# Performance work log

Hardware: AMD Instinct MI355X
Metric: run time of the kernel (lower is better)

Reference implementation:

```python
import jax, jax.numpy as jnp
from jax import lax
import numpy as np

HH = WW = 128          # backbone feature map (2048px image / stride 16)
C_IN = 512
FEAT_STRIDE = 16
N_ANCHOR = 9
NMS_THRESH = 0.7
N_PRE_NMS = 6000
N_POST_NMS = 300
MIN_SIZE = 16
NEG = jnp.float32(-1e30)


def _anchor_base(base_size=16, ratios=(0.5, 1.0, 2.0), scales=(8, 16, 32)):
    py = px = base_size / 2.0
    ab = np.zeros((len(ratios) * len(scales), 4), np.float32)
    for i, r in enumerate(ratios):
        for j, s in enumerate(scales):
            h = base_size * s * np.sqrt(r)
            w = base_size * s * np.sqrt(1.0 / r)
            ab[i * len(scales) + j] = [py - h / 2, px - w / 2, py + h / 2, px + w / 2]
    return ab


def _shifted_anchors(hh, ww):
    # (y1, x1, y2, x2) anchors enumerated row-major over (y, x), anchors innermost
    ab = _anchor_base()
    sy = np.arange(0, hh * FEAT_STRIDE, FEAT_STRIDE, dtype=np.float32)
    sx = np.arange(0, ww * FEAT_STRIDE, FEAT_STRIDE, dtype=np.float32)
    sx, sy = np.meshgrid(sx, sy)
    shift = np.stack((sy.ravel(), sx.ravel(), sy.ravel(), sx.ravel()), axis=1)
    anc = (ab[None, :, :] + shift[:, None, :]).reshape(-1, 4)
    return jnp.asarray(anc)


def _conv(x, w, b):
    y = lax.conv_general_dilated(x, w, (1, 1), 'SAME',
                                 dimension_numbers=('NHWC', 'HWIO', 'NHWC'))
    return y + b


def _loc2bbox(anchor, loc):
    sh = anchor[:, 2] - anchor[:, 0]
    sw = anchor[:, 3] - anchor[:, 1]
    scy = anchor[:, 0] + 0.5 * sh
    scx = anchor[:, 1] + 0.5 * sw
    cy = loc[:, 0] * sh + scy
    cx = loc[:, 1] * sw + scx
    h = jnp.exp(loc[:, 2]) * sh
    w = jnp.exp(loc[:, 3]) * sw
    return jnp.stack([cy - 0.5 * h, cx - 0.5 * w, cy + 0.5 * h, cx + 0.5 * w], axis=1)


def _nms(boxes, scores, thresh, n_out):
    # Greedy NMS with a fixed output size; invalid slots are zeroed.
    y1, x1, y2, x2 = boxes[:, 0], boxes[:, 1], boxes[:, 2], boxes[:, 3]
    areas = (y2 - y1) * (x2 - x1)

    def step(valid, _):
        s = jnp.where(valid, scores, NEG)
        i = jnp.argmax(s)
        ok = s[i] > NEG
        iy1 = jnp.maximum(y1, y1[i]); ix1 = jnp.maximum(x1, x1[i])
        iy2 = jnp.minimum(y2, y2[i]); ix2 = jnp.minimum(x2, x2[i])
        inter = jnp.maximum(iy2 - iy1, 0.0) * jnp.maximum(ix2 - ix1, 0.0)
        iou = inter / (areas + areas[i] - inter + 1e-9)
        valid = valid & (iou <= thresh)  # picked box suppresses itself (iou=1)
        return valid, (i, ok)

    _, (idx, oks) = lax.scan(step, jnp.ones(scores.shape, bool), None, length=n_out)
    return boxes[idx] * oks[:, None].astype(boxes.dtype)


def _proposals(loc, fg_score, anchor, img_h, img_w, scale):
    dst = _loc2bbox(anchor, loc)
    dst = jnp.stack([jnp.clip(dst[:, 0], 0.0, img_h),
                     jnp.clip(dst[:, 1], 0.0, img_w),
                     jnp.clip(dst[:, 2], 0.0, img_h),
                     jnp.clip(dst[:, 3], 0.0, img_w)], axis=1)
    min_size = MIN_SIZE * scale
    hs = dst[:, 2] - dst[:, 0]
    ws = dst[:, 3] - dst[:, 1]
    keep = (hs >= min_size) & (ws >= min_size)
    sc = jnp.where(keep, fg_score, -jnp.inf)
    top_s, top_i = lax.top_k(sc, N_PRE_NMS)
    return _nms(dst[top_i], top_s, NMS_THRESH, N_POST_NMS)


def _rpn_forward(x, conv_w, conv_b, loc_w, loc_b, score_w, score_b, img_h, img_w, scale):
    n, hh, ww, _ = x.shape
    anchor = _shifted_anchors(hh, ww)                    # [hh*ww*9, 4]
    h = jax.nn.relu(_conv(x, conv_w, conv_b))            # [n, hh, ww, 512]
    rpn_loc = _conv(h, loc_w, loc_b).reshape(n, -1, 4)   # [n, hh*ww*9, 4]
    rpn_score_map = _conv(h, score_w, score_b)           # [n, hh, ww, 18]
    soft = jax.nn.softmax(rpn_score_map.reshape(n, hh, ww, N_ANCHOR, 2), axis=-1)
    rpn_fg = soft[..., 1].reshape(n, -1)                 # [n, hh*ww*9]
    rpn_score = rpn_score_map.reshape(n, -1, 2)
    roi = _proposals(rpn_loc[0], rpn_fg[0], anchor, img_h, img_w, scale)  # [300, 4]
    return rpn_loc, rpn_score, roi, anchor


def setup_inputs() -> dict:
    key = jax.random.key(0)
    ks = jax.random.split(key, 4)
    return {
        "x": jax.random.normal(ks[0], (1, HH, WW, C_IN), jnp.float32),
        "conv_w": jax.random.normal(ks[1], (3, 3, C_IN, 512), jnp.float32) * 0.02,
        "conv_b": jnp.zeros((512,), jnp.float32),
        "loc_w": jax.random.normal(ks[2], (1, 1, 512, 36), jnp.float32) * 0.02,
        "loc_b": jnp.zeros((36,), jnp.float32),
        "score_w": jax.random.normal(ks[3], (1, 1, 512, 18), jnp.float32) * 0.02,
        "score_b": jnp.zeros((18,), jnp.float32),
        "img_h": HH * FEAT_STRIDE,
        "img_w": WW * FEAT_STRIDE,
        "scale": 1,
    }


def reference(x, conv_w, conv_b, loc_w, loc_b, score_w, score_b, img_h, img_w, scale):
    return _rpn_forward(x, conv_w, conv_b, loc_w, loc_b, score_w, score_b,
                        float(img_h), float(img_w), float(scale))
```

## Files before the change

### kernel.cpp

```cpp
#include <hip/hip_runtime.h>
#include <math.h>

typedef unsigned int u32;
typedef unsigned long long u64;
typedef _Float16 half8 __attribute__((ext_vector_type(8)));
typedef float f32x4 __attribute__((ext_vector_type(4)));
typedef float f32x16 __attribute__((ext_vector_type(16)));

#define N_PIX 16384
#define N_ANC 147456
#define N_PRE 6000
#define TIE_BASE 6144
#define TIE_CAP  16384

#define OFF_H      0ULL
#define OFF_BOXES  33554432ULL
#define OFF_KEYS   35913728ULL
#define OFF_W54    36503552ULL
#define OFF_B54    36634624ULL
#define OFF_HIST1  36634880ULL
#define OFF_HIST2  36897024ULL
#define OFF_CTRL   37159168ULL
#define OFF_CAND   37159424ULL
#define OFF_SBOX   37339648ULL
#define OFF_MASK   37437952ULL
#define BASE_NEEDED 41961984ULL
#define OFF_XH     41961984ULL
#define OFF_XL     58739200ULL
#define OFF_WHT    75516416ULL
#define OFF_WLT    80235008ULL
#define FULL_NEEDED 84953600ULL

#define KEY_NEGINF 0x007FFFFFu

#define MASK_BYTES 4524032ULL

struct AB { float v[36]; };


__device__ __forceinline__ void d_init_body(int i0, u32* hist1, u32* hist2, u32* ctrl, float* roi,
                       float* w54, float* b54,
                       const float* __restrict__ loc_w, const float* __restrict__ loc_b,
                       const float* __restrict__ score_w, const float* __restrict__ score_b) {
  const int stride = 256 * 256;
  const int TOT = 65536 * 2 + 64 + 1200 + 32768 + 64;
  for (int i = i0; i < TOT; i += stride) {
    if (i < 65536) hist1[i] = 0u;
    else if (i < 131072) hist2[i - 65536] = 0u;
    else if (i < 131136) ctrl[i - 131072] = 0u;
    else if (i < 132336) roi[i - 131136] = 0.f;
    else if (i < 165104) {
      int j = i - 132336;
      int k = j >> 6, oc = j & 63;
      float v = 0.f;
      if (oc < 36) v = loc_w[k * 36 + oc];
      else if (oc < 54) v = score_w[k * 18 + oc - 36];
      w54[(((k >> 2) << 6) + oc) * 4 + (k & 3)] = v;
    } else {
      int oc = i - 165104;
      float v = 0.f;
      if (oc < 36) v = loc_b[oc];
      else if (oc < 54) v = score_b[oc - 36];
      b54[oc] = v;
    }
  }
}

__device__ __forceinline__ void d_split_x_body(int b, int t, const float* __restrict__ x,
                                               _Float16* __restrict__ xh, _Float16* __restrict__ xl) {
  const int gid = b * 256 + t;
  const int base = gid << 3;
  float a[8];
  *(float4*)&a[0] = *(const float4*)(x + base);
  *(float4*)&a[4] = *(const float4*)(x + base + 4);
  half8 hh, ll;
#pragma unroll
  for (int j = 0; j < 8; ++j) {
    _Float16 hi = (_Float16)a[j];
    hh[j] = hi;
    ll[j] = (_Float16)((a[j] - (float)hi) * 2048.0f);
  }
  *(half8*)(xh + base) = hh;
  *(half8*)(xl + base) = ll;
}

__device__ __forceinline__ void d_split_w_body(int kb64, int ob, int t, const float* __restrict__ w,
                                               _Float16* __restrict__ whPK, _Float16* __restrict__ wlPK,
                                               _Float16 (*th)[72], _Float16 (*tl)[72]) {
  {
    const int r = t >> 2, cq = t & 3;
    float a[16];
    const float* wp = w + ((size_t)(kb64 * 64 + r) << 9) + ob * 64 + cq * 16;
#pragma unroll
    for (int j = 0; j < 4; ++j) *(float4*)&a[j << 2] = *(const float4*)(wp + (j << 2));
    half8 h0, h1, l0, l1;
#pragma unroll
    for (int j = 0; j < 8; ++j) {
      _Float16 hi = (_Float16)a[j];
      h0[j] = hi; l0[j] = (_Float16)((a[j] - (float)hi) * 2048.0f);
    }
#pragma unroll
    for (int j = 0; j < 8; ++j) {
      _Float16 hi = (_Float16)a[8 + j];
      h1[j] = hi; l1[j] = (_Float16)((a[8 + j] - (float)hi) * 2048.0f);
    }
    *(half8*)&th[r][cq * 16]     = h0;
    *(half8*)&th[r][cq * 16 + 8] = h1;
    *(half8*)&tl[r][cq * 16]     = l0;
    *(half8*)&tl[r][cq * 16 + 8] = l1;
  }
  __syncthreads();
  {
    const int o_local = t & 63;
    const int hl = (t >> 6) & 1;
    const int cs = t >> 7;
    const int tap = kb64 >> 3;
    const int ci  = ((kb64 & 7) << 1) + cs;
    const int kb  = ci * 9 + tap;
    const int o   = ob * 64 + o_local;
    const int nb  = o >> 7, n = o & 127;
    _Float16* dst = (hl ? wlPK : whPK) + (((size_t)(nb * 144 + kb) << 7) + n) * 32;
    _Float16 (*src)[72] = hl ? tl : th;
    const int r0 = cs << 5;
    half8 v0, v1, v2, v3;
#pragma unroll
    for (int j = 0; j < 8; ++j) {
      v0[j] = src[r0 + j][o_local];
      v1[j] = src[r0 + 8 + j][o_local];
      v2[j] = src[r0 + 16 + j][o_local];
      v3[j] = src[r0 + 24 + j][o_local];
    }
    *(half8*)(dst)      = v0;
    *(half8*)(dst + 8)  = v1;
    *(half8*)(dst + 16) = v2;
    *(half8*)(dst + 24) = v3;
  }
}

__global__ void k_init(u32* hist1, u32* hist2, u32* ctrl, float* roi,
                       float* w54, float* b54,
                       const float* __restrict__ loc_w, const float* __restrict__ loc_b,
                       const float* __restrict__ score_w, const float* __restrict__ score_b) {
  const int i0 = blockIdx.x * blockDim.x + threadIdx.x;
  d_init_body(i0, hist1, hist2, ctrl, roi, w54, b54, loc_w, loc_b, score_w, score_b);
}

__global__ __launch_bounds__(256) void k_prep(const float* __restrict__ x,
                                              _Float16* __restrict__ xh, _Float16* __restrict__ xl,
                                              const float* __restrict__ w,
                                              _Float16* __restrict__ whPK, _Float16* __restrict__ wlPK,
                                              u32* hist1, u32* hist2, u32* ctrl, float* roi,
                                              float* w54, float* b54,
                                              const float* __restrict__ loc_w, const float* __restrict__ loc_b,
                                              const float* __restrict__ score_w, const float* __restrict__ score_b) {
  __shared__ _Float16 th[64][72];
  __shared__ _Float16 tl[64][72];
  const int b = blockIdx.x;
  const int t = threadIdx.x;
  if (b < 4096) {
    d_split_x_body(b, t, x, xh, xl);
  } else if (b < 4672) {
    const int idx = b - 4096;
    d_split_w_body(idx % 72, idx / 72, t, w, whPK, wlPK, th, tl);
  } else {
    d_init_body((b - 4672) * 256 + t, hist1, hist2, ctrl, roi, w54, b54, loc_w, loc_b, score_w, score_b);
  }
}

__global__ __launch_bounds__(256, 2) void k_conv_pre(const _Float16* __restrict__ xh,
                                                     const _Float16* __restrict__ xl,
                                                     const _Float16* __restrict__ whPK,
                                                     const _Float16* __restrict__ wlPK,
                                                     const float* __restrict__ bias,
                                                     float* __restrict__ h) {
  __shared__ _Float16 As[2][2][4][128][8];

  const int bid = blockIdx.x;
  const int q   = bid >> 3;
  const int nb  = q >> 4;
  const int y   = ((bid & 7) << 4) + (q & 15);

  const int t  = threadIdx.x;
  const int wv = t >> 6, lane = t & 63;
  const int m0 = (wv >> 1) << 6;
  const int n0 = (wv & 1) << 6;
  const int ln5 = lane & 31;
  const int kh  = lane >> 5;

  const int s_m = t >> 1;
  const int kq0 = (t & 1) << 1;
  const int ch0 = kq0 << 3;

  f32x16 acc_hh[2][2];
  f32x16 acc_x[2][2];
#pragma unroll
  for (int i = 0; i < 2; ++i)
#pragma unroll
    for (int j = 0; j < 2; ++j) { acc_hh[i][j] = (f32x16)0.f; acc_x[i][j] = (f32x16)0.f; }

  const int ct0 = (s_m - 1) << 9;
  const int ct1 = s_m << 9;
  const int ct2 = (s_m + 1) << 9;
  const bool cok0 = (s_m >= 1);
  const bool cok2 = (s_m <= 126);

  const u32 wcol = (((u32)(n0 + ln5)) << 5) + ((u32)kh << 3);

  half8 rah0, rah1, ral0, ral1;
  half8 bh0[2][2], bl0[2][2], bh1[2][2], bl1[2][2];

#define CONV_LOADA(KB)                                                           \
  {                                                                              \
    const int ci_   = (KB) / 9;                                                  \
    const int tap_  = (KB) - ci_ * 9;                                            \
    const int ky_   = tap_ / 3, kx_ = tap_ - ky_ * 3;                            \
    const int cin0_ = ci_ << 5;                                                  \
    const int yy_   = y + ky_ - 1;                                               \
    const bool rok_ = (yy_ >= 0) && (yy_ < 128);                                 \
    const int colterm_ = (kx_ == 0) ? ct0 : ((kx_ == 1) ? ct1 : ct2);            \
    const bool cok_    = (kx_ == 0) ? cok0 : ((kx_ == 1) ? true : cok2);         \
    if (rok_ && cok_) {                                                          \
      const u32 aoff_ = (u32)((yy_ << 16) + cin0_ + ch0 + colterm_);             \
      rah0 = *(const half8*)(xh + aoff_);                                        \
      rah1 = *(const half8*)(xh + aoff_ + 8);                                    \
      ral0 = *(const half8*)(xl + aoff_);                                        \
      ral1 = *(const half8*)(xl + aoff_ + 8);                                    \
    } else {                                                                     \
      rah0 = (half8)(_Float16)0; rah1 = (half8)(_Float16)0;                      \
      ral0 = (half8)(_Float16)0; ral1 = (half8)(_Float16)0;                      \
    }                                                                            \
  }

#define CONV_STOREA(BUF)                                                         \
  {                                                                              \
    *(half8*)As[BUF][0][kq0][s_m]     = rah0;                                    \
    *(half8*)As[BUF][0][kq0 + 1][s_m] = rah1;                                    \
    *(half8*)As[BUF][1][kq0][s_m]     = ral0;                                    \
    *(half8*)As[BUF][1][kq0 + 1][s_m] = ral1;                                    \
  }

#define BLOAD(KB, BH, BL)                                                        \
  {                                                                              \
    const u32 kbase_ = ((u32)(nb * 144 + (KB))) << 12;    \
    _Pragma("unroll")                                                            \
    for (int i_ = 0; i_ < 2; ++i_) {                                             \
      _Pragma("unroll")                                                          \
      for (int ks_ = 0; ks_ < 2; ++ks_) {                                        \
        const u32 o_ = kbase_ + wcol + ((u32)i_ << 10) + ((u32)ks_ << 4);        \
        BH[i_][ks_] = *(const half8*)(whPK + o_);                                \
        BL[i_][ks_] = *(const half8*)(wlPK + o_);                                \
      }                                                                          \
    }                                                                            \
  }

#define FRAGSA(KS, AH, AL)                                                       \
  {                                                                              \
    const int kq_ = ((KS) << 1) + kh;                                            \
    _Pragma("unroll")                                                            \
    for (int i = 0; i < 2; ++i) {                                                \
      AH[i] = *(const half8*)As[cur][0][kq_][m0 + (i << 5) + ln5];               \
      AL[i] = *(const half8*)As[cur][1][kq_][m0 + (i << 5) + ln5];               \
    }                                                                            \
  }

#define MFMA6(AH, AL, BH, BL, KS)                                                \
  {                                                                              \
    _Pragma("unroll")                                                            \
    for (int mi = 0; mi < 2; ++mi)                                               \
      _Pragma("unroll")                                                          \
      for (int ni = 0; ni < 2; ++ni) {                                           \
        acc_hh[mi][ni] = __builtin_amdgcn_mfma_f32_32x32x16_f16(AH[mi], BH[ni][KS], acc_hh[mi][ni], 0, 0, 0); \
        acc_x[mi][ni]  = __builtin_amdgcn_mfma_f32_32x32x16_f16(AH[mi], BL[ni][KS], acc_x[mi][ni], 0, 0, 0);  \
        acc_x[mi][ni]  = __builtin_amdgcn_mfma_f32_32x32x16_f16(AL[mi], BH[ni][KS], acc_x[mi][ni], 0, 0, 0);  \
      }                                                                          \
  }

  CONV_LOADA(0);
  BLOAD(0, bh0, bl0);
  CONV_STOREA(0);
  __syncthreads();

  int cur = 0;
#pragma unroll 1
  for (int kb = 0; kb < 144; kb += 2) {
    {
      half8 a0h[2], a0l[2], a1h[2], a1l[2];
      FRAGSA(0, a0h, a0l);
      CONV_LOADA(kb + 1);
      BLOAD(kb + 1, bh1, bl1);
      __builtin_amdgcn_sched_barrier(0);
      __builtin_amdgcn_s_setprio(1);
      MFMA6(a0h, a0l, bh0, bl0, 0);
      __builtin_amdgcn_s_setprio(0);
      FRAGSA(1, a1h, a1l);
      __builtin_amdgcn_s_setprio(1);
      MFMA6(a1h, a1l, bh0, bl0, 1);
      __builtin_amdgcn_s_setprio(0);
      CONV_STOREA(cur ^ 1);
      __syncthreads();
      cur ^= 1;
    }
    {
      half8 a0h[2], a0l[2], a1h[2], a1l[2];
      FRAGSA(0, a0h, a0l);
      if (kb + 2 < 144) {
        CONV_LOADA(kb + 2);
        BLOAD(kb + 2, bh0, bl0);
      }
      __builtin_amdgcn_sched_barrier(0);
      __builtin_amdgcn_s_setprio(1);
      MFMA6(a0h, a0l, bh1, bl1, 0);
      __builtin_amdgcn_s_setprio(0);
      FRAGSA(1, a1h, a1l);
      __builtin_amdgcn_s_setprio(1);
      MFMA6(a1h, a1l, bh1, bl1, 1);
      __builtin_amdgcn_s_setprio(0);
      if (kb + 2 < 144) {
        CONV_STOREA(cur ^ 1);
        __syncthreads();
        cur ^= 1;
      }
    }
  }
#undef CONV_LOADA
#undef CONV_STOREA
#undef BLOAD
#undef FRAGSA
#undef MFMA6

  const float inv2048 = 1.0f / 2048.0f;
#pragma unroll
  for (int mi = 0; mi < 2; ++mi)
#pragma unroll
    for (int ni = 0; ni < 2; ++ni) {
      const int col = n0 + (ni << 5) + ln5;
      const float bbv = bias[(nb << 7) + col];
#pragma unroll
      for (int r = 0; r < 16; ++r) {
        const int row = m0 + (mi << 5) + (r & 3) + ((r >> 2) << 3) + (kh << 2);
        float v = acc_hh[mi][ni][r] + acc_x[mi][ni][r] * inv2048 + bbv;
        h[(((size_t)((y << 7) + row)) << 9) + (nb << 7) + col] = fmaxf(v, 0.f);
      }
    }
}

#define APAD 40
__global__ __launch_bounds__(256, 2) void k_conv_fb(const float* __restrict__ x,
                                                    const float* __restrict__ w,
                                                    const float* __restrict__ bias,
                                                    float* __restrict__ h) {
  __shared__ _Float16 Ah[128][APAD];
  __shared__ _Float16 Al[128][APAD];
  __shared__ _Float16 Bh[128][APAD];
  __shared__ _Float16 Bl[128][APAD];

  const int y  = blockIdx.x;
  const int nb = blockIdx.y;
  const int t  = threadIdx.x;
  const int wv = t >> 6, lane = t & 63;
  const int m0 = (wv >> 1) << 6;
  const int n0 = (wv & 1) << 6;
  const int fm = lane & 15;
  const int fq = lane >> 4;
  const int sa_m = t >> 1;
  const int sa_h = (t & 1) << 4;
  const int sb_n = t & 127;
  const int sb_kg = (t >> 7) << 4;

  f32x4 acc_hh[4][4];
  f32x4 acc_x[4][4];
#pragma unroll
  for (int i = 0; i < 4; ++i)
#pragma unroll
    for (int j = 0; j < 4; ++j) { acc_hh[i][j] = (f32x4)0.f; acc_x[i][j] = (f32x4)0.f; }

#pragma unroll 1
  for (int kb = 0; kb < 144; ++kb) {
    const int tap  = kb >> 4;
    const int ky   = tap / 3, kx = tap - ky * 3;
    const int cin0 = (kb & 15) << 5;
    {
      const int yy = y + ky - 1;
      const int xx = sa_m + kx - 1;
      float av[16];
      if (yy >= 0 && yy < 128 && xx >= 0 && xx < 128) {
        const float* ap = x + (((size_t)((yy << 7) + xx)) << 9) + cin0 + sa_h;
#pragma unroll
        for (int j = 0; j < 4; ++j) *(float4*)&av[j << 2] = *(const float4*)(ap + (j << 2));
      } else {
#pragma unroll
        for (int j = 0; j < 16; ++j) av[j] = 0.f;
      }
      half8 h0, h1, l0, l1;
#pragma unroll
      for (int j = 0; j < 8; ++j) {
        _Float16 hi = (_Float16)av[j];
        h0[j] = hi; l0[j] = (_Float16)((av[j] - (float)hi) * 2048.0f);
      }
#pragma unroll
      for (int j = 0; j < 8; ++j) {
        _Float16 hi = (_Float16)av[8 + j];
        h1[j] = hi; l1[j] = (_Float16)((av[8 + j] - (float)hi) * 2048.0f);
      }
      *(half8*)&Ah[sa_m][sa_h]     = h0;
      *(half8*)&Ah[sa_m][sa_h + 8] = h1;
      *(half8*)&Al[sa_m][sa_h]     = l0;
      *(half8*)&Al[sa_m][sa_h + 8] = l1;
    }
    {
      const float* bp = w + ((size_t)(tap * 512 + cin0 + sb_kg) << 9) + (nb << 7) + sb_n;
      float bv[16];
#pragma unroll
      for (int j = 0; j < 16; ++j) bv[j] = bp[(size_t)j << 9];
      half8 h0, h1, l0, l1;
#pragma unroll
      for (int j = 0; j < 8; ++j) {
        _Float16 hi = (_Float16)bv[j];
        h0[j] = hi; l0[j] = (_Float16)((bv[j] - (float)hi) * 2048.0f);
      }
#pragma unroll
      for (int j = 0; j < 8; ++j) {
        _Float16 hi = (_Float16)bv[8 + j];
        h1[j] = hi; l1[j] = (_Float16)((bv[8 + j] - (float)hi) * 2048.0f);
      }
      *(half8*)&Bh[sb_n][sb_kg]     = h0;
      *(half8*)&Bh[sb_n][sb_kg + 8] = h1;
      *(half8*)&Bl[sb_n][sb_kg]     = l0;
      *(half8*)&Bl[sb_n][sb_kg + 8] = l1;
    }
    __syncthreads();
    half8 ah[4], al[4], bh[4], bl[4];
#pragma unroll
    for (int i = 0; i < 4; ++i) {
      ah[i] = *(const half8*)&Ah[m0 + (i << 4) + fm][fq << 3];
      al[i] = *(const half8*)&Al[m0 + (i << 4) + fm][fq << 3];
      bh[i] = *(const half8*)&Bh[n0 + (i << 4) + fm][fq << 3];
      bl[i] = *(const half8*)&Bl[n0 + (i << 4) + fm][fq << 3];
    }
#pragma unroll
    for (int mi = 0; mi < 4; ++mi)
#pragma unroll
      for (int ni = 0; ni < 4; ++ni) {
        acc_hh[mi][ni] = __builtin_amdgcn_mfma_f32_16x16x32_f16(ah[mi], bh[ni], acc_hh[mi][ni], 0, 0, 0);
        acc_x[mi][ni]  = __builtin_amdgcn_mfma_f32_16x16x32_f16(ah[mi], bl[ni], acc_x[mi][ni], 0, 0, 0);
        acc_x[mi][ni]  = __builtin_amdgcn_mfma_f32_16x16x32_f16(al[mi], bh[ni], acc_x[mi][ni], 0, 0, 0);
      }
    __syncthreads();
  }
  const float inv2048 = 1.0f / 2048.0f;
#pragma unroll
  for (int mi = 0; mi < 4; ++mi)
#pragma unroll
    for (int ni = 0; ni < 4; ++ni) {
      const int col = n0 + (ni << 4) + fm;
      const float bb = bias[(nb << 7) + col];
#pragma unroll
      for (int r = 0; r < 4; ++r) {
        const int row = m0 + (mi << 4) + (fq << 2) + r;
        float v = acc_hh[mi][ni][r] + acc_x[mi][ni][r] * inv2048 + bb;
        h[(((size_t)((y << 7) + row)) << 9) + (nb << 7) + col] = fmaxf(v, 0.f);
      }
    }
}

__global__ __launch_bounds__(256) void k_heads(const float* __restrict__ h,
        const float4* __restrict__ w54, const float* __restrict__ b54,
        float* __restrict__ out0, float* __restrict__ out1, float* __restrict__ out3,
        float4* __restrict__ boxes, u32* __restrict__ keys, u32* __restrict__ hist1,
        const int* __restrict__ p_ih, const int* __restrict__ p_iw,
        const int* __restrict__ p_sc, AB ab) {
  __shared__ float hl[16 * 512];
  __shared__ float vals[16][64];
  const int t = threadIdx.x;
  const int wv = t >> 6, lane = t & 63;
  const int pbase = blockIdx.x << 4;

#pragma unroll
  for (int j = 0; j < 8; ++j) {
    const int f = (j << 8) + t;
    ((float4*)hl)[f] = ((const float4*)(h + ((size_t)pbase << 9)))[f];
  }
  __syncthreads();

  const float* hp = hl + ((wv << 2) << 9);
  float a0 = 0.f, a1 = 0.f, a2 = 0.f, a3 = 0.f;
#pragma unroll 4
  for (int kq = 0; kq < 128; ++kq) {
    const float4 wvv = w54[(kq << 6) + lane];
    const float4 h0 = *(const float4*)(hp + (kq << 2));
    const float4 h1 = *(const float4*)(hp + 512 + (kq << 2));
    const float4 h2 = *(const float4*)(hp + 1024 + (kq << 2));
    const float4 h3 = *(const float4*)(hp + 1536 + (kq << 2));
    a0 += h0.x * wvv.x + h0.y * wvv.y + h0.z * wvv.z + h0.w * wvv.w;
    a1 += h1.x * wvv.x + h1.y * wvv.y + h1.z * wvv.z + h1.w * wvv.w;
    a2 += h2.x * wvv.x + h2.y * wvv.y + h2.z * wvv.z + h2.w * wvv.w;
    a3 += h3.x * wvv.x + h3.y * wvv.y + h3.z * wvv.z + h3.w * wvv.w;
  }
  const float bb = b54[lane];
  float av[4] = {a0 + bb, a1 + bb, a2 + bb, a3 + bb};
#pragma unroll
  for (int px = 0; px < 4; ++px) {
    const int p = pbase + (wv << 2) + px;
    vals[(wv << 2) + px][lane] = av[px];
    if (lane < 36) out0[p * 36 + lane] = av[px];
    else if (lane < 54) out1[p * 18 + lane - 36] = av[px];
  }
  __syncthreads();

  if (lane < 36) {
    const int px = lane / 9, a = lane - px * 9;
    const int p = pbase + (wv << 2) + px;
    const float* vv = vals[(wv << 2) + px];
    const float l0 = vv[(a << 2) + 0], l1 = vv[(a << 2) + 1];
    const float l2 = vv[(a << 2) + 2], l3 = vv[(a << 2) + 3];
    const float s0 = vv[36 + (a << 1)], s1 = vv[37 + (a << 1)];
    const int yq = p >> 7, xq = p & 127;
    const float fy = (float)(yq << 4), fx = (float)(xq << 4);
    const float ay1 = ab.v[(a << 2) + 0] + fy;
    const float ax1 = ab.v[(a << 2) + 1] + fx;
    const float ay2 = ab.v[(a << 2) + 2] + fy;
    const float ax2 = ab.v[(a << 2) + 3] + fx;
    const int idx = p * 9 + a;
    *(float4*)(out3 + ((size_t)idx << 2)) = make_float4(ay1, ax1, ay2, ax2);

    const float sh = ay2 - ay1, sw = ax2 - ax1;
    const float scy = ay1 + 0.5f * sh, scx = ax1 + 0.5f * sw;
    const float cy = l0 * sh + scy, cx = l1 * sw + scx;
    const float bh = expf(l2) * sh, bw = expf(l3) * sw;
    const float IH = (float)p_ih[0], IW = (float)p_iw[0];
    float d0 = fminf(fmaxf(cy - 0.5f * bh, 0.f), IH);
    float d1 = fminf(fmaxf(cx - 0.5f * bw, 0.f), IW);
    float d2 = fminf(fmaxf(cy + 0.5f * bh, 0.f), IH);
    float d3 = fminf(fmaxf(cx + 0.5f * bw, 0.f), IW);
    boxes[idx] = make_float4(d0, d1, d2, d3);

    const float minsz = 16.f * (float)p_sc[0];
    const bool keep = (d2 - d0 >= minsz) && (d3 - d1 >= minsz);
    const float mx = fmaxf(s0, s1);
    const float e0 = expf(s0 - mx), e1 = expf(s1 - mx);
    const float fg = e1 / (e0 + e1);
    const float sc = keep ? fg : -INFINITY;
    const u32 u = __float_as_uint(sc);
    const u32 key = (u & 0x80000000u) ? ~u : (u | 0x80000000u);
    keys[idx] = key;
    atomicAdd(&hist1[key >> 16], 1u);
  }
}

__global__ void k_hist2(const u32* __restrict__ keys, const u32* __restrict__ ctrl,
                        u32* __restrict__ hist2) {
  const u32 b1 = ctrl[0];
  int i = blockIdx.x * blockDim.x + threadIdx.x;
  if (i < N_ANC) {
    const u32 k = keys[i];
    if ((k >> 16) == b1) atomicAdd(&hist2[k & 0xFFFFu], 1u);
  }
}

__global__ __launch_bounds__(1024) void k_findcut(const u32* __restrict__ hist,
                                                  u32* __restrict__ ctrl, int mode) {
  __shared__ u32 csum[1024];
  __shared__ u32 suf[1024];
  const int t = threadIdx.x;
  const u32 target = (mode == 0) ? (u32)N_PRE : ((u32)N_PRE - ctrl[1]);
  const int base = t << 6;
  u32 s = 0;
  for (int i = 0; i < 64; ++i) s += hist[base + i];
  csum[t] = s;
  suf[t] = s;
  __syncthreads();
  for (int off = 1; off < 1024; off <<= 1) {
    u32 add = (t + off < 1024) ? suf[t + off] : 0u;
    __syncthreads();
    suf[t] += add;
    __syncthreads();
  }
  const u32 excl = suf[t] - csum[t];
  if (excl < target && target <= suf[t]) {
    u32 cum = excl;
    int bkt = base;
    for (int i = 63; i >= 0; --i) {
      const u32 hh = hist[base + i];
      if (cum < target && target <= cum + hh) { bkt = base + i; break; }
      cum += hh;
    }
    if (mode == 0) { ctrl[0] = (u32)bkt; ctrl[1] = cum; }
    else {
      const u32 Kstar = (ctrl[0] << 16) | (u32)bkt;
      const u32 A = ctrl[1] + cum;
      u32 need = (u32)N_PRE - A;
      if (Kstar == KEY_NEGINF) need = 0u;
      ctrl[2] = Kstar; ctrl[3] = A; ctrl[4] = need;
      ctrl[7] = A + need;
    }
  }
}

__global__ void k_compact(const u32* __restrict__ keys, u32* __restrict__ ctrl,
                          u64* __restrict__ cand) {
  const u32 Kstar = ctrl[2];
  const u32 need  = ctrl[4];
  int i = blockIdx.x * blockDim.x + threadIdx.x;
  if (i >= N_ANC) return;
  const u32 k = keys[i];
  if (k > Kstar) {
    const u32 pos = atomicAdd(&ctrl[5], 1u);
    cand[pos] = ((u64)k << 32) | (u64)(u32)(~(u32)i);
  } else if (k == Kstar && need != 0u) {
    const u32 pos = atomicAdd(&ctrl[6], 1u);
    if (pos < (u32)TIE_CAP) cand[TIE_BASE + pos] = ((u64)Kstar << 32) | (u64)(u32)(~(u32)i);
  }
}

__global__ __launch_bounds__(128) void k_rank(const u32* __restrict__ ctrl,
                                              const u64* __restrict__ cand,
                                              const float4* __restrict__ boxes,
                                              float4* __restrict__ sbox) {
  __shared__ u32 wred[2];
  const u32 A   = ctrl[3];
  const u32 tcc = min(ctrl[6], (u32)TIE_CAP);
  const u32 C   = A + tcc;
  const u32 L   = ctrl[7];
  const int t   = threadIdx.x;
  for (u32 i = blockIdx.x; i < C; i += gridDim.x) {
    const u64 v = (i < A) ? cand[i] : cand[TIE_BASE + (i - A)];
    u32 cnt = 0;
    for (u32 j = t; j < A; j += 128) cnt += (cand[j] > v);
    for (u32 j = t; j < tcc; j += 128) cnt += (cand[TIE_BASE + j] > v);
#pragma unroll
    for (int off = 32; off > 0; off >>= 1) cnt += __shfl_xor(cnt, off);
    if ((t & 63) == 0) wred[t >> 6] = cnt;
    __syncthreads();
    if (t == 0) {
      const u32 rank = wred[0] + wred[1];
      if (rank < L) {
        const u32 idx = ~((u32)(v & 0xFFFFFFFFULL));
        sbox[rank] = boxes[idx];
      }
    }
    __syncthreads();
  }
}

__global__ __launch_bounds__(256) void k_mask(const u32* __restrict__ ctrl,
                                              const float4* __restrict__ sbox,
                                              u64* __restrict__ mask) {
  const int L = (int)ctrl[7];
  const int rb = blockIdx.y;
  if (rb * 64 >= L) return;
  const int wv = threadIdx.x >> 6;
  const int lane = threadIdx.x & 63;
  const int cw = (blockIdx.x << 2) + wv;
  if (cw > 93 || cw < rb) return;
  const int j = cw * 64 + lane;
  const bool jok = (j < L);
  const float4 cb = jok ? sbox[j] : make_float4(0.f, 0.f, 0.f, 0.f);
  const float careaJ = (cb.z - cb.x) * (cb.w - cb.y);
  const int rbase = rb * 64;
  const float4 rbx = (rbase + lane < L) ? sbox[rbase + lane] : make_float4(0.f, 0.f, 0.f, 0.f);
  const int rmax = min(64, L - rbase);
  for (int r = 0; r < rmax; ++r) {
    const float ry1 = __shfl(rbx.x, r), rx1 = __shfl(rbx.y, r);
    const float ry2 = __shfl(rbx.z, r), rx2 = __shfl(rbx.w, r);
    const float ra = (ry2 - ry1) * (rx2 - rx1);
    const float iy1 = fmaxf(cb.x, ry1), ix1 = fmaxf(cb.y, rx1);
    const float iy2 = fminf(cb.z, ry2), ix2 = fminf(cb.w, rx2);
    const float inter = fmaxf(iy2 - iy1, 0.f) * fmaxf(ix2 - ix1, 0.f);
    const float iou = inter / (careaJ + ra - inter + 1e-9f);
    const bool bit = jok && (iou > 0.7f);
    const u64 bal = __ballot(bit);
    if (lane == 0) mask[(size_t)(rbase + r) * 94 + cw] = bal;
  }
}

__device__ inline u64 valid_mask_fn(int base, int L) {
  const int r = L - base;
  if (r <= 0) return 0ULL;
  if (r >= 64) return ~0ULL;
  return (1ULL << r) - 1ULL;
}
__device__ inline u64 above_mask_fn(int base, int i) {
  if (i < base) return ~0ULL;
  const int s = i - base + 1;
  if (s >= 64) return 0ULL;
  return (~0ULL) << s;
}

__device__ __forceinline__ void gload_lds16(const void* g, void* l) {
  __builtin_amdgcn_global_load_lds(
      (const __attribute__((address_space(1))) void*)g,
      (__attribute__((address_space(3))) void*)l, 16, 0, 0);
}

__global__ __launch_bounds__(64) void k_greedy(const u32* __restrict__ ctrl,
                                               const float* __restrict__ sboxf,
                                               const u64* __restrict__ mask,
                                               float* __restrict__ roi) {
  __shared__ char lds[4 * 12288];
  const int lane = threadIdx.x;
  const int L = (int)ctrl[7];
  if (L <= 0) return;
  const char* gmask = (const char*)mask;
  const char* gend  = gmask + MASK_BYTES;
  const int nbatch = (L + 15) >> 4;

#define GISSUE(BB)                                                         \
  {                                                                        \
    const char* gb_ = gmask + (size_t)(BB) * 12032;                        \
    char* lb_ = lds + ((BB) & 3) * 12288;                                  \
    _Pragma("unroll")                                                      \
    for (int j_ = 0; j_ < 12; ++j_) {                                      \
      const char* ga_ = gb_ + j_ * 1024;                                   \
      if (ga_ + 1024 > gend) ga_ = gend - 1024;    \
      gload_lds16(ga_ + lane * 16, lb_ + j_ * 1024);                       \
    }                                                                      \
  }

  int next_issue = 0;
  int ready = -1;
  const int base0 = lane << 6;
  const int base1 = (64 + lane) << 6;
  const u64 v0 = valid_mask_fn(base0, L);
  const u64 v1 = (lane < 30) ? valid_mask_fn(base1, L) : 0ULL;
  u64 rem0 = 0ULL, rem1 = 0ULL;
  int i = 0, kept = 0;

  while (i >= 0 && kept < 300) {
    const int bi = i >> 4;
    if (bi > ready) {
      if (next_issue < bi) next_issue = bi;
      const int want = min(bi + 3, nbatch - 1);
      while (next_issue <= want) { GISSUE(next_issue); ++next_issue; }
      const int out = next_issue - 1 - bi;
      if (out >= 3)      asm volatile("s_waitcnt vmcnt(36)" ::: "memory");
      else if (out == 2) asm volatile("s_waitcnt vmcnt(24)" ::: "memory");
      else if (out == 1) asm volatile("s_waitcnt vmcnt(12)" ::: "memory");
      else               asm volatile("s_waitcnt vmcnt(0)"  ::: "memory");
      ready = bi;
    }
    if (lane < 4) roi[kept * 4 + lane] = sboxf[(size_t)i * 4 + lane];
    ++kept;
    const u64* rowp = (const u64*)(lds + (bi & 3) * 12288 + (i & 15) * 752);
    rem0 |= rowp[lane];
    if (lane < 30) rem1 |= rowp[64 + lane];
    const u64 f0 = ~rem0 & v0 & above_mask_fn(base0, i);
    const u64 f1 = ~rem1 & v1 & above_mask_fn(base1, i);
    int ni = -1;
    const u64 b0 = __ballot(f0 != 0ULL);
    if (b0) {
      const int w = (int)__builtin_ctzll(b0);
      const u64 fw = (u64)__shfl((long long)f0, w);
      ni = (w << 6) + (int)__builtin_ctzll(fw);
    } else {
      const u64 b1m = __ballot(f1 != 0ULL);
      if (b1m) {
        const int w = (int)__builtin_ctzll(b1m);
        const u64 fw = (u64)__shfl((long long)f1, w);
        ni = ((64 + w) << 6) + (int)__builtin_ctzll(fw);
      }
    }
    i = ni;
  }
#undef GISSUE
}

extern "C" void kernel_launch(void* const* d_in, const int* in_sizes, int n_in,
                              void* d_out, int out_size, void* d_ws, size_t ws_size,
                              hipStream_t stream) {
  (void)in_sizes; (void)n_in; (void)out_size;
  if (ws_size < BASE_NEEDED) return;
  const bool fast = (ws_size >= FULL_NEEDED);

  const float* x       = (const float*)d_in[0];
  const float* conv_w  = (const float*)d_in[1];
  const float* conv_b  = (const float*)d_in[2];
  const float* loc_w   = (const float*)d_in[3];
  const float* loc_b   = (const float*)d_in[4];
  const float* score_w = (const float*)d_in[5];
  const float* score_b = (const float*)d_in[6];
  const int* p_ih = (const int*)d_in[7];
  const int* p_iw = (const int*)d_in[8];
  const int* p_sc = (const int*)d_in[9];

  float* out0 = (float*)d_out;
  float* out1 = out0 + 589824;
  float* roi  = out1 + 294912;
  float* out3 = roi + 1200;

  char* ws = (char*)d_ws;
  float*     h     = (float*)(ws + OFF_H);
  float4*    boxes = (float4*)(ws + OFF_BOXES);
  u32*       keys  = (u32*)(ws + OFF_KEYS);
  float*     w54   = (float*)(ws + OFF_W54);
  float*     b54   = (float*)(ws + OFF_B54);
  u32*       hist1 = (u32*)(ws + OFF_HIST1);
  u32*       hist2 = (u32*)(ws + OFF_HIST2);
  u32*       ctrl  = (u32*)(ws + OFF_CTRL);
  u64*       cand  = (u64*)(ws + OFF_CAND);
  float4*    sbox  = (float4*)(ws + OFF_SBOX);
  u64*       mask  = (u64*)(ws + OFF_MASK);
  _Float16*  xh    = (_Float16*)(ws + OFF_XH);
  _Float16*  xl    = (_Float16*)(ws + OFF_XL);
  _Float16*  whPK  = (_Float16*)(ws + OFF_WHT);
  _Float16*  wlPK  = (_Float16*)(ws + OFF_WLT);

  AB ab;
  {
    const double ratios[3] = {0.5, 1.0, 2.0};
    const double scales[3] = {8.0, 16.0, 32.0};
    for (int i = 0; i < 3; ++i)
      for (int j = 0; j < 3; ++j) {
        const double hh = 16.0 * scales[j] * sqrt(ratios[i]);
        const double wwv = 16.0 * scales[j] * sqrt(1.0 / ratios[i]);
        const int a = i * 3 + j;
        ab.v[a * 4 + 0] = (float)(8.0 - hh / 2.0);
        ab.v[a * 4 + 1] = (float)(8.0 - wwv / 2.0);
        ab.v[a * 4 + 2] = (float)(8.0 + hh / 2.0);
        ab.v[a * 4 + 3] = (float)(8.0 + wwv / 2.0);
      }
  }

  if (fast) {
    hipLaunchKernelGGL(k_prep, dim3(4928), dim3(256), 0, stream,
                       x, xh, xl, conv_w, whPK, wlPK,
                       hist1, hist2, ctrl, roi, w54, b54, loc_w, loc_b, score_w, score_b);
    hipLaunchKernelGGL(k_conv_pre, dim3(512), dim3(256), 0, stream, xh, xl, whPK, wlPK, conv_b, h);
  } else {
    hipLaunchKernelGGL(k_init, dim3(256), dim3(256), 0, stream,
                       hist1, hist2, ctrl, roi, w54, b54, loc_w, loc_b, score_w, score_b);
    hipLaunchKernelGGL(k_conv_fb, dim3(128, 4), dim3(256), 0, stream, x, conv_w, conv_b, h);
  }
  hipLaunchKernelGGL(k_heads, dim3(1024), dim3(256), 0, stream,
                     h, (const float4*)w54, b54, out0, out1, out3, boxes, keys, hist1,
                     p_ih, p_iw, p_sc, ab);
  hipLaunchKernelGGL(k_findcut, dim3(1), dim3(1024), 0, stream, hist1, ctrl, 0);
  hipLaunchKernelGGL(k_hist2, dim3(576), dim3(256), 0, stream, keys, ctrl, hist2);
  hipLaunchKernelGGL(k_findcut, dim3(1), dim3(1024), 0, stream, hist2, ctrl, 1);
  hipLaunchKernelGGL(k_compact, dim3(576), dim3(256), 0, stream, keys, ctrl, cand);
  hipLaunchKernelGGL(k_rank, dim3(8192), dim3(128), 0, stream, ctrl, cand, boxes, sbox);
  hipLaunchKernelGGL(k_mask, dim3(24, 94), dim3(256), 0, stream, ctrl, sbox, mask);
  hipLaunchKernelGGL(k_greedy, dim3(1), dim3(64), 0, stream, ctrl, (const float*)sbox, mask, roi);
}
```

Before: 667.9 us.

## Repack conv weights for coalesced B loads and use LDS-only barriers

Changes the packed fp16 hi/lo weight layout so that each k-quarter forms a contiguous 1024-element plane, with 8-half groups indexed by output column. Consecutive lanes in the MFMA B-fragment loads then read adjacent 16-byte chunks instead of 64-byte strided ones. The prep kernel's store pattern and the conv's BLOAD addressing are updated together to match. It also replaces __syncthreads with an explicit lgkmcnt(0) wait plus s_barrier, so the barrier does not wait on the outstanding global loads that prefetch the next block. That wait is only safe if no pending global stores or loads must complete before the barrier; here only LDS writes need ordering.

```diff
diff --git a/kernel.cpp b/kernel.cpp
--- a/kernel.cpp
+++ b/kernel.cpp
@@ -119,21 +119,16 @@
     const int kb  = ci * 9 + tap;
     const int o   = ob * 64 + o_local;
     const int nb  = o >> 7, n = o & 127;
-    _Float16* dst = (hl ? wlPK : whPK) + (((size_t)(nb * 144 + kb) << 7) + n) * 32;
+    _Float16* dst = (hl ? wlPK : whPK) + (((size_t)(nb * 144 + kb)) << 12) + n * 8;
     _Float16 (*src)[72] = hl ? tl : th;
     const int r0 = cs << 5;
-    half8 v0, v1, v2, v3;
-#pragma unroll
-    for (int j = 0; j < 8; ++j) {
-      v0[j] = src[r0 + j][o_local];
-      v1[j] = src[r0 + 8 + j][o_local];
-      v2[j] = src[r0 + 16 + j][o_local];
-      v3[j] = src[r0 + 24 + j][o_local];
-    }
-    *(half8*)(dst)      = v0;
-    *(half8*)(dst + 8)  = v1;
-    *(half8*)(dst + 16) = v2;
-    *(half8*)(dst + 24) = v3;
+#pragma unroll
+    for (int q = 0; q < 4; ++q) {
+      half8 v;
+#pragma unroll
+      for (int j = 0; j < 8; ++j) v[j] = src[r0 + (q << 3) + j][o_local];
+      *(half8*)(dst + (q << 10)) = v;
+    }
   }
 }
 
@@ -204,7 +199,7 @@
   const bool cok0 = (s_m >= 1);
   const bool cok2 = (s_m <= 126);
 
-  const u32 wcol = (((u32)(n0 + ln5)) << 5) + ((u32)kh << 3);
+  const u32 wb = ((u32)kh << 10) + (((u32)(n0 + ln5)) << 3);
 
   half8 rah0, rah1, ral0, ral1;
   half8 bh0[2][2], bl0[2][2], bh1[2][2], bl1[2][2];
@@ -246,7 +241,7 @@
     for (int i_ = 0; i_ < 2; ++i_) {                                             \
       _Pragma("unroll")                                                          \
       for (int ks_ = 0; ks_ < 2; ++ks_) {                                        \
-        const u32 o_ = kbase_ + wcol + ((u32)i_ << 10) + ((u32)ks_ << 4);        \
+        const u32 o_ = kbase_ + ((u32)ks_ << 11) + wb + ((u32)i_ << 8);          \
         BH[i_][ks_] = *(const half8*)(whPK + o_);                                \
         BL[i_][ks_] = *(const half8*)(wlPK + o_);                                \
       }                                                                          \
@@ -275,10 +270,16 @@
       }                                                                          \
   }
 
+#define LBARRIER()                                                               \
+  {                                                                              \
+    asm volatile("s_waitcnt lgkmcnt(0)" ::: "memory");                           \
+    __builtin_amdgcn_s_barrier();                                                \
+  }
+
   CONV_LOADA(0);
   BLOAD(0, bh0, bl0);
   CONV_STOREA(0);
-  __syncthreads();
+  LBARRIER();
 
   int cur = 0;
 #pragma unroll 1
@@ -297,7 +298,7 @@
       MFMA6(a1h, a1l, bh0, bl0, 1);
       __builtin_amdgcn_s_setprio(0);
       CONV_STOREA(cur ^ 1);
-      __syncthreads();
+      LBARRIER();
       cur ^= 1;
     }
     {
@@ -317,7 +318,7 @@
       __builtin_amdgcn_s_setprio(0);
       if (kb + 2 < 144) {
         CONV_STOREA(cur ^ 1);
-        __syncthreads();
+        LBARRIER();
         cur ^= 1;
       }
     }
@@ -327,6 +328,7 @@
 #undef BLOAD
 #undef FRAGSA
 #undef MFMA6
+#undef LBARRIER
 
   const float inv2048 = 1.0f / 2048.0f;
 #pragma unroll
```

Measured after the change: 653.2 us. 1.02x faster.
